# Kernel optimization log

Measured on AMD Instinct MI355X. Metric: run time of the kernel, lower is better.

Reference implementation:

```python
import jax, jax.numpy as jnp
import numpy as np

START_TAG = 2
STOP_TAG = 3
NEG = -10000.0


def _lstm_dir(x, w_ih, w_hh, b_ih, b_hh, h0, c0):
    """Single-direction LSTM over x:[T,F]. PyTorch gate order i,f,g,o."""
    xp = x @ w_ih.T + b_ih  # [T, 4H] - big GEMM done once

    def step(carry, xt):
        h, c = carry
        g = xt + h @ w_hh.T + b_hh
        i, f, gg, o = jnp.split(g, 4)
        c = jax.nn.sigmoid(f) * c + jax.nn.sigmoid(i) * jnp.tanh(gg)
        h = jax.nn.sigmoid(o) * jnp.tanh(c)
        return (h, c), h

    _, hs = jax.lax.scan(step, (h0, c0), xp)
    return hs  # [T, H]


def _viterbi(feats, transitions):
    # feats: [T, n_tags]; transitions[next, prev]
    n = transitions.shape[0]
    init = jnp.full((n,), NEG, feats.dtype).at[START_TAG].set(0.0)

    def step(fv, feat):
        scores = fv[None, :] + transitions          # [next, prev]
        bptr = jnp.argmax(scores, axis=1)           # best prev per next
        return jnp.max(scores, axis=1) + feat, bptr

    fv, bptrs = jax.lax.scan(step, init, feats)
    terminal = fv + transitions[STOP_TAG]
    best = jnp.argmax(terminal)
    score = terminal[best]

    def back(tag, bp):
        return bp[tag], tag  # emit tag at step t, carry tag at t-1

    _, path = jax.lax.scan(back, best, bptrs, reverse=True)
    return score, path  # scalar, [T] int32


def setup_inputs() -> dict:
    key = jax.random.key(0)
    T, F, H = 4096, 1024, 2048
    H2 = H // 2
    NTAG = 4
    ks = jax.random.split(key, 16)
    s_ih = 1.0 / np.sqrt(H2)

    def u(k, shape, s):
        return jax.random.uniform(k, shape, jnp.float32, -s, s)

    transitions = jax.random.normal(ks[13], (NTAG, NTAG), jnp.float32)
    transitions = transitions.at[START_TAG, :].set(NEG)
    transitions = transitions.at[:, STOP_TAG].set(NEG)

    return {
        "sentence": jax.random.normal(ks[0], (T, F), jnp.float32),
        "h0": jax.random.normal(ks[1], (2, 1, H2), jnp.float32),
        "c0": jax.random.normal(ks[2], (2, 1, H2), jnp.float32),
        "w_ih_f": u(ks[3], (4 * H2, F), s_ih),
        "w_hh_f": u(ks[4], (4 * H2, H2), s_ih),
        "b_ih_f": u(ks[5], (4 * H2,), s_ih),
        "b_hh_f": u(ks[6], (4 * H2,), s_ih),
        "w_ih_b": u(ks[7], (4 * H2, F), s_ih),
        "w_hh_b": u(ks[8], (4 * H2, H2), s_ih),
        "b_ih_b": u(ks[9], (4 * H2,), s_ih),
        "b_hh_b": u(ks[10], (4 * H2,), s_ih),
        "w_tag": u(ks[11], (NTAG, H), 1.0 / np.sqrt(H)),
        "b_tag": u(ks[12], (NTAG,), 1.0 / np.sqrt(H)),
        "transitions": transitions,
    }


def reference(sentence, h0, c0, w_ih_f, w_hh_f, b_ih_f, b_hh_f,
              w_ih_b, w_hh_b, b_ih_b, b_hh_b, w_tag, b_tag, transitions):
    # Bidirectional LSTM, batch=1 (torch stacks directions on dim 0 of h0/c0)
    h_fwd = _lstm_dir(sentence, w_ih_f, w_hh_f, b_ih_f, b_hh_f, h0[0, 0], c0[0, 0])
    h_bwd = _lstm_dir(sentence[::-1], w_ih_b, w_hh_b, b_ih_b, b_hh_b, h0[1, 0], c0[1, 0])[::-1]
    lstm_out = jnp.concatenate([h_fwd, h_bwd], axis=-1)  # [T, hidden_dim]
    feats = lstm_out @ w_tag.T + b_tag                    # [T, 4]
    score, path = _viterbi(feats, transitions)
    return score, path
```

## Files before the change

### kernel.cpp

```cpp
#include <hip/hip_runtime.h>
#include <cstddef>
#include <cstdint>

#define T_LEN 4096
#define FDIM  1024
#define H2DIM 1024
#define GDIM  4096

#define NEGV (-10000.0f)
#define START_TAG 2
#define STOP_TAG 3

#define XP_OFF      ((size_t)0)
#define XP_BYTES    ((size_t)2 * T_LEN * GDIM * 4)
#define HIST_OFF    (XP_OFF + XP_BYTES)
#define HIST_BYTES  ((size_t)T_LEN * 2048 * 4)
#define FEATS_OFF   (HIST_OFF + HIST_BYTES)
#define FEATS_BYTES ((size_t)T_LEN * 4 * 4)
#define SLOTS_OFF   (FEATS_OFF + FEATS_BYTES)
#define SLOTS_BYTES ((size_t)2 * 2 * 1024 * 8)
#define WS_NEED     (SLOTS_OFF + SLOTS_BYTES)

#define XB_OFF      (HIST_OFF)
#define WBF_OFF     (HIST_OFF + (size_t)8  * 1024 * 1024)
#define WBB_OFF     (HIST_OFF + (size_t)16 * 1024 * 1024)

__device__ __forceinline__ float sigm(float x) { return 1.0f / (1.0f + expf(-x)); }

__device__ __forceinline__ unsigned short f2bf(float f) {
    unsigned u = __float_as_uint(f);
    return (unsigned short)((u + 0x7FFFu + ((u >> 16) & 1u)) >> 16);
}

__device__ __forceinline__ unsigned compose4(unsigned A, unsigned B) {
    unsigned r = 0;
    #pragma unroll
    for (int c = 0; c < 4; ++c) {
        const unsigned b = (B >> (8 * c)) & 3u;
        const unsigned a = (A >> (8 * b)) & 3u;
        r |= a << (8 * c);
    }
    return r;
}

typedef short  bf16x8 __attribute__((ext_vector_type(8)));
typedef float  f32x4  __attribute__((ext_vector_type(4)));

__global__ __launch_bounds__(256)
void conv_bf16(const float* __restrict__ src, unsigned short* __restrict__ dst, int n4)
{
    int i = blockIdx.x * 256 + threadIdx.x;
    const int stride = gridDim.x * 256;
    for (; i < n4; i += stride) {
        const float4 v = ((const float4*)src)[i];
        ushort4 o;
        o.x = f2bf(v.x); o.y = f2bf(v.y); o.z = f2bf(v.z); o.w = f2bf(v.w);
        ((ushort4*)dst)[i] = o;
    }
}

__global__ __launch_bounds__(64)
void xp_gemm_mfma(const unsigned short* __restrict__ xb,
                  const unsigned short* __restrict__ wb_f,
                  const unsigned short* __restrict__ wb_b,
                  const float* __restrict__ bi_f, const float* __restrict__ bh_f,
                  const float* __restrict__ bi_b, const float* __restrict__ bh_b,
                  float* __restrict__ xp)
{
    const int lane = threadIdx.x;
    const int j0   = blockIdx.x * 64;
    const int t0   = blockIdx.y * 64;
    const int dir  = blockIdx.z;
    const unsigned short* __restrict__ wb = dir ? wb_b : wb_f;
    const float* __restrict__ bi = dir ? bi_b : bi_f;
    const float* __restrict__ bh = dir ? bh_b : bh_f;

    const int r  = lane & 15;
    const int kg = lane >> 4;

    const unsigned short* arow[4];
    const unsigned short* brow[4];
    #pragma unroll
    for (int s = 0; s < 4; ++s) {
        const int tg = t0 + s * 16 + r;
        const int sr = dir ? (T_LEN - 1 - tg) : tg;
        arow[s] = xb + (size_t)sr * FDIM + kg * 8;
        brow[s] = wb + (size_t)(j0 + s * 16 + r) * FDIM + kg * 8;
    }

    f32x4 acc[4][4];
    #pragma unroll
    for (int sm = 0; sm < 4; ++sm)
        #pragma unroll
        for (int sn = 0; sn < 4; ++sn)
            acc[sm][sn] = (f32x4){0.f, 0.f, 0.f, 0.f};

    for (int k0 = 0; k0 < FDIM; k0 += 32) {
        bf16x8 a[4], b[4];
        #pragma unroll
        for (int s = 0; s < 4; ++s) {
            a[s] = *(const bf16x8*)(arow[s] + k0);
            b[s] = *(const bf16x8*)(brow[s] + k0);
        }
        #pragma unroll
        for (int sm = 0; sm < 4; ++sm)
            #pragma unroll
            for (int sn = 0; sn < 4; ++sn)
                acc[sm][sn] = __builtin_amdgcn_mfma_f32_16x16x32_bf16(
                                  a[sm], b[sn], acc[sm][sn], 0, 0, 0);
    }

    float* __restrict__ xpd = xp + (size_t)dir * T_LEN * GDIM;
    #pragma unroll
    for (int sn = 0; sn < 4; ++sn) {
        const int col  = j0 + sn * 16 + r;
        const float bv = bi[col] + bh[col];
        #pragma unroll
        for (int sm = 0; sm < 4; ++sm) {
            #pragma unroll
            for (int j = 0; j < 4; ++j) {
                const int row = t0 + sm * 16 + kg * 4 + j;
                xpd[(size_t)row * GDIM + col] = acc[sm][sn][j] + bv;
            }
        }
    }
}

__global__ __launch_bounds__(256, 1)
void lstm_scan(const float* __restrict__ xp,
               const float* __restrict__ h0,
               const float* __restrict__ c0,
               const float* __restrict__ whh_f,
               const float* __restrict__ whh_b,
               float* __restrict__ hist,
               unsigned long long* __restrict__ slots)
{
    __shared__ float wsl[32][1024];
    __shared__ float hbuf[1024];
    __shared__ float gsh[32];

    const int tid = threadIdx.x;
    const int b   = blockIdx.x;
    const int dir = b & 1;
    const int bi  = b >> 1;
    const int u0  = bi * 8;
    const int rg  = tid >> 5;
    const int kc  = tid & 31;
    const int lrb = rg * 4;

    const float* __restrict__ whh = dir ? whh_b : whh_f;
    const size_t xpbase = (size_t)dir * T_LEN * GDIM;

    for (int lr = 0; lr < 32; ++lr) {
        const int grow = ((lr >> 3) << 10) + u0 + (lr & 7);
        *(float4*)&wsl[lr][tid * 4] = *(const float4*)&whh[(size_t)grow * H2DIM + tid * 4];
    }
    *(float4*)&hbuf[tid * 4] = *(const float4*)&h0[dir * H2DIM + tid * 4];
    float creg = 0.f;
    if (tid < 8) creg = c0[dir * H2DIM + u0 + tid];

    int grows[4];
    #pragma unroll
    for (int j = 0; j < 4; ++j) {
        const int lr = lrb + j;
        grows[j] = ((lr >> 3) << 10) + u0 + (lr & 7);
    }
    float xpc[4] = {0.f, 0.f, 0.f, 0.f};
    if (kc == 0) {
        #pragma unroll
        for (int j = 0; j < 4; ++j) xpc[j] = xp[xpbase + grows[j]];
    }
    __syncthreads();

    int budget = 4000000;

    for (int t = 0; t < T_LEN; ++t) {
        float xpn[4] = {0.f, 0.f, 0.f, 0.f};
        const int tnx = (t + 1 < T_LEN) ? (t + 1) : t;
        if (kc == 0) {
            #pragma unroll
            for (int j = 0; j < 4; ++j) xpn[j] = xp[xpbase + (size_t)tnx * GDIM + grows[j]];
        }

        float p0 = 0.f, p1 = 0.f, p2 = 0.f, p3 = 0.f;
        #pragma unroll
        for (int s = 0; s < 8; ++s) {
            const int ko = s * 128 + kc * 4;
            const float4 hv = *(const float4*)&hbuf[ko];
            const float4 w0 = *(const float4*)&wsl[lrb + 0][ko];
            const float4 w1 = *(const float4*)&wsl[lrb + 1][ko];
            const float4 w2 = *(const float4*)&wsl[lrb + 2][ko];
            const float4 w3 = *(const float4*)&wsl[lrb + 3][ko];
            p0 += w0.x*hv.x + w0.y*hv.y + w0.z*hv.z + w0.w*hv.w;
            p1 += w1.x*hv.x + w1.y*hv.y + w1.z*hv.z + w1.w*hv.w;
            p2 += w2.x*hv.x + w2.y*hv.y + w2.z*hv.z + w2.w*hv.w;
            p3 += w3.x*hv.x + w3.y*hv.y + w3.z*hv.z + w3.w*hv.w;
        }
        #pragma unroll
        for (int m = 16; m >= 1; m >>= 1) {
            p0 += __shfl_xor(p0, m);
            p1 += __shfl_xor(p1, m);
            p2 += __shfl_xor(p2, m);
            p3 += __shfl_xor(p3, m);
        }
        if (kc == 0) {
            gsh[lrb + 0] = p0 + xpc[0];
            gsh[lrb + 1] = p1 + xpc[1];
            gsh[lrb + 2] = p2 + xpc[2];
            gsh[lrb + 3] = p3 + xpc[3];
        }
        __syncthreads();

        if (tid < 8) {
            const float gi = gsh[tid];
            const float gf = gsh[8 + tid];
            const float gg = gsh[16 + tid];
            const float go = gsh[24 + tid];
            const float c  = sigm(gf) * creg + sigm(gi) * tanhf(gg);
            const float h  = sigm(go) * tanhf(c);
            creg = c;
            const int tg = dir ? (T_LEN - 1 - t) : t;
            hist[(size_t)tg * 2048 + dir * H2DIM + u0 + tid] = h;
            const unsigned long long pack =
                ((unsigned long long)(unsigned)(t + 1) << 32) |
                (unsigned long long)__float_as_uint(h);
            __hip_atomic_store(&slots[((size_t)((t + 1) & 1) * 2 + dir) * H2DIM + u0 + tid],
                               pack, __ATOMIC_RELAXED, __HIP_MEMORY_SCOPE_AGENT);
        }

        if (t + 1 < T_LEN) {
            const unsigned want = (unsigned)(t + 1);
            unsigned long long* sb = &slots[((size_t)((t + 1) & 1) * 2 + dir) * H2DIM + tid * 4];
            unsigned long long v0 = 0, v1 = 0, v2 = 0, v3 = 0;
            bool g0 = false, g1 = false, g2 = false, g3 = false;
            for (;;) {
                if (!g0) v0 = __hip_atomic_load(&sb[0], __ATOMIC_RELAXED, __HIP_MEMORY_SCOPE_AGENT);
                if (!g1) v1 = __hip_atomic_load(&sb[1], __ATOMIC_RELAXED, __HIP_MEMORY_SCOPE_AGENT);
                if (!g2) v2 = __hip_atomic_load(&sb[2], __ATOMIC_RELAXED, __HIP_MEMORY_SCOPE_AGENT);
                if (!g3) v3 = __hip_atomic_load(&sb[3], __ATOMIC_RELAXED, __HIP_MEMORY_SCOPE_AGENT);
                g0 = g0 || ((unsigned)(v0 >> 32) == want);
                g1 = g1 || ((unsigned)(v1 >> 32) == want);
                g2 = g2 || ((unsigned)(v2 >> 32) == want);
                g3 = g3 || ((unsigned)(v3 >> 32) == want);
                if (g0 && g1 && g2 && g3) break;
                if (--budget <= 0) break;
                __builtin_amdgcn_s_sleep(1);
            }
            float4 hv;
            hv.x = __uint_as_float((unsigned)v0);
            hv.y = __uint_as_float((unsigned)v1);
            hv.z = __uint_as_float((unsigned)v2);
            hv.w = __uint_as_float((unsigned)v3);
            *(float4*)&hbuf[tid * 4] = hv;
        }
        __syncthreads();
        if (kc == 0) { xpc[0] = xpn[0]; xpc[1] = xpn[1]; xpc[2] = xpn[2]; xpc[3] = xpn[3]; }
    }
}

__global__ __launch_bounds__(256)
void feats_kernel(const float* __restrict__ hist,
                  const float* __restrict__ w_tag,
                  const float* __restrict__ b_tag,
                  float* __restrict__ feats)
{
    const int t = blockIdx.x;
    const int tid = threadIdx.x;
    const float* __restrict__ hrow = hist + (size_t)t * 2048 + tid * 8;
    const float4 ha = *(const float4*)&hrow[0];
    const float4 hb = *(const float4*)&hrow[4];
    float p[4];
    #pragma unroll
    for (int n = 0; n < 4; ++n) {
        const float* __restrict__ wr = w_tag + n * 2048 + tid * 8;
        const float4 wa = *(const float4*)&wr[0];
        const float4 wb = *(const float4*)&wr[4];
        p[n] = ha.x*wa.x + ha.y*wa.y + ha.z*wa.z + ha.w*wa.w
             + hb.x*wb.x + hb.y*wb.y + hb.z*wb.z + hb.w*wb.w;
    }
    #pragma unroll
    for (int m = 32; m >= 1; m >>= 1) {
        #pragma unroll
        for (int n = 0; n < 4; ++n) p[n] += __shfl_down(p[n], m);
    }
    __shared__ float red[4][4];
    const int wv = tid >> 6;
    if ((tid & 63) == 0) {
        #pragma unroll
        for (int n = 0; n < 4; ++n) red[n][wv] = p[n];
    }
    __syncthreads();
    if (tid < 4)
        feats[(size_t)t * 4 + tid] = red[tid][0] + red[tid][1] + red[tid][2] + red[tid][3] + b_tag[tid];
}

__global__ __launch_bounds__(256)
void viterbi_kernel(const float* __restrict__ feats,
                    const float* __restrict__ trans,
                    float* __restrict__ out)
{
    __shared__ float fsh[T_LEN * 4];
    __shared__ unsigned bp[T_LEN];
    __shared__ unsigned lmap[256];
    __shared__ unsigned smap[256];
    __shared__ int bestsh;
    const int tid = threadIdx.x;
    for (int i = tid; i < T_LEN; i += 256)
        *(float4*)&fsh[i * 4] = *(const float4*)&feats[(size_t)i * 4];
    __syncthreads();

    if (tid == 0) {
        float tr[16];
        #pragma unroll
        for (int i = 0; i < 16; ++i) tr[i] = trans[i];
        float fv[4] = {NEGV, NEGV, NEGV, NEGV};
        fv[START_TAG] = 0.0f;
        for (int t0 = 0; t0 < T_LEN; t0 += 8) {
            float4 f8[8];
            #pragma unroll
            for (int j = 0; j < 8; ++j) f8[j] = *(const float4*)&fsh[(t0 + j) * 4];
            #pragma unroll
            for (int j = 0; j < 8; ++j) {
                const float ft[4] = {f8[j].x, f8[j].y, f8[j].z, f8[j].w};
                float nf[4]; unsigned pb = 0;
                #pragma unroll
                for (int n = 0; n < 4; ++n) {
                    float m = fv[0] + tr[n * 4 + 0]; int bsel = 0;
                    #pragma unroll
                    for (int p = 1; p < 4; ++p) {
                        const float s = fv[p] + tr[n * 4 + p];
                        if (s > m) { m = s; bsel = p; }
                    }
                    nf[n] = m + ft[n];
                    pb |= (unsigned)bsel << (8 * n);
                }
                bp[t0 + j] = pb;
                fv[0] = nf[0]; fv[1] = nf[1]; fv[2] = nf[2]; fv[3] = nf[3];
            }
        }
        float bm = fv[0] + tr[STOP_TAG * 4 + 0]; int best = 0;
        #pragma unroll
        for (int p = 1; p < 4; ++p) {
            const float s = fv[p] + tr[STOP_TAG * 4 + p];
            if (s > bm) { bm = s; best = p; }
        }
        out[0] = bm;
        bestsh = best;
    }
    __syncthreads();

    const int c0 = tid * 16;
    unsigned L = bp[c0 + 15];
    #pragma unroll
    for (int j = 14; j >= 0; --j) L = compose4(bp[c0 + j], L);
    lmap[tid] = L;
    __syncthreads();
    if (tid == 0) {
        unsigned acc = 0x03020100u;
        for (int i = 255; i >= 0; --i) { smap[i] = acc; acc = compose4(lmap[i], acc); }
    }
    __syncthreads();
    unsigned carry = smap[tid];
    const int best = bestsh;
    for (int t = c0 + 15; t >= c0; --t) {
        out[1 + t] = (float)((carry >> (8 * best)) & 3u);
        carry = compose4(bp[t], carry);
    }
}

extern "C" void kernel_launch(void* const* d_in, const int* in_sizes, int n_in,
                              void* d_out, int out_size, void* d_ws, size_t ws_size,
                              hipStream_t stream) {
    const float* x      = (const float*)d_in[0];
    const float* h0     = (const float*)d_in[1];
    const float* c0     = (const float*)d_in[2];
    const float* w_ih_f = (const float*)d_in[3];
    const float* w_hh_f = (const float*)d_in[4];
    const float* b_ih_f = (const float*)d_in[5];
    const float* b_hh_f = (const float*)d_in[6];
    const float* w_ih_b = (const float*)d_in[7];
    const float* w_hh_b = (const float*)d_in[8];
    const float* b_ih_b = (const float*)d_in[9];
    const float* b_hh_b = (const float*)d_in[10];
    const float* w_tag  = (const float*)d_in[11];
    const float* b_tag  = (const float*)d_in[12];
    const float* trans  = (const float*)d_in[13];
    float* out = (float*)d_out;

    if (ws_size < WS_NEED) return;

    char* ws = (char*)d_ws;
    float* xp    = (float*)(ws + XP_OFF);
    float* hist  = (float*)(ws + HIST_OFF);
    float* feats = (float*)(ws + FEATS_OFF);
    unsigned long long* slots = (unsigned long long*)(ws + SLOTS_OFF);
    unsigned short* xb  = (unsigned short*)(ws + XB_OFF);
    unsigned short* wbf = (unsigned short*)(ws + WBF_OFF);
    unsigned short* wbb = (unsigned short*)(ws + WBB_OFF);

    hipMemsetAsync(slots, 0, SLOTS_BYTES, stream);

    const int n4 = (T_LEN * FDIM) / 4;
    conv_bf16<<<1024, 256, 0, stream>>>(x,      xb,  n4);
    conv_bf16<<<1024, 256, 0, stream>>>(w_ih_f, wbf, n4);
    conv_bf16<<<1024, 256, 0, stream>>>(w_ih_b, wbb, n4);

    xp_gemm_mfma<<<dim3(64, 64, 2), 64, 0, stream>>>(
        xb, wbf, wbb, b_ih_f, b_hh_f, b_ih_b, b_hh_b, xp);

    void* ka[] = { (void*)&xp, (void*)&h0, (void*)&c0, (void*)&w_hh_f, (void*)&w_hh_b,
                   (void*)&hist, (void*)&slots };
    hipLaunchCooperativeKernel((void*)lstm_scan, dim3(256), dim3(256), ka, 0, stream);

    feats_kernel<<<T_LEN, 256, 0, stream>>>(hist, w_tag, b_tag, feats);
    viterbi_kernel<<<1, 256, 0, stream>>>(feats, trans, out);
}
```

Baseline: 14.01 ms.

## Tile input-projection GEMM through LDS with 128x128 blocks and block swizzle

The bf16 MFMA GEMM for the input projection now uses 256-thread blocks computing 128x128 tiles, staging A and B k-slices in padded shared memory so that four waves share the loaded data. Before, each 64-thread block read its operands directly from global memory. A swizzled block index groups neighbouring tiles to improve L2 reuse. The cost is two barriers per k-step with no double buffering, and the GEMM is a small part of a runtime dominated by the sequential LSTM scan.

Result: no change. 13.80 ms (-1.5%).

```diff
diff --git a/kernel.cpp b/kernel.cpp
--- a/kernel.cpp
+++ b/kernel.cpp
@@ -59,7 +59,7 @@
     }
 }
 
-__global__ __launch_bounds__(64)
+__global__ __launch_bounds__(256)
 void xp_gemm_mfma(const unsigned short* __restrict__ xb,
                   const unsigned short* __restrict__ wb_f,
                   const unsigned short* __restrict__ wb_b,
@@ -67,10 +67,21 @@
                   const float* __restrict__ bi_b, const float* __restrict__ bh_b,
                   float* __restrict__ xp)
 {
-    const int lane = threadIdx.x;
-    const int j0   = blockIdx.x * 64;
-    const int t0   = blockIdx.y * 64;
-    const int dir  = blockIdx.z;
+    __shared__ unsigned short As[128][40];
+    __shared__ unsigned short Bs[128][40];
+
+    const int tid  = threadIdx.x;
+    const int lane = tid & 63;
+    const int wv   = tid >> 6;
+    const int wr   = (wv >> 1) * 64;
+    const int wc   = (wv & 1) * 64;
+    const int dir  = blockIdx.y;
+
+    const int bid = blockIdx.x;
+    const int swz = (bid & 7) * 128 + (bid >> 3);
+    const int t0  = (swz >> 5) * 128;
+    const int j0  = (swz & 31) * 128;
+
     const unsigned short* __restrict__ wb = dir ? wb_b : wb_f;
     const float* __restrict__ bi = dir ? bi_b : bi_f;
     const float* __restrict__ bh = dir ? bh_b : bh_f;
@@ -78,15 +89,15 @@
     const int r  = lane & 15;
     const int kg = lane >> 4;
 
-    const unsigned short* arow[4];
-    const unsigned short* brow[4];
-    #pragma unroll
-    for (int s = 0; s < 4; ++s) {
-        const int tg = t0 + s * 16 + r;
-        const int sr = dir ? (T_LEN - 1 - tg) : tg;
-        arow[s] = xb + (size_t)sr * FDIM + kg * 8;
-        brow[s] = wb + (size_t)(j0 + s * 16 + r) * FDIM + kg * 8;
-    }
+    const int srow = tid >> 2;
+    const int skp  = (tid & 3) * 8;
+
+    const int tgA0 = t0 + srow;
+    const int tgA1 = t0 + srow + 64;
+    const size_t arow0 = (size_t)(dir ? (T_LEN - 1 - tgA0) : tgA0) * FDIM;
+    const size_t arow1 = (size_t)(dir ? (T_LEN - 1 - tgA1) : tgA1) * FDIM;
+    const size_t brow0 = (size_t)(j0 + srow) * FDIM;
+    const size_t brow1 = (size_t)(j0 + srow + 64) * FDIM;
 
     f32x4 acc[4][4];
     #pragma unroll
@@ -95,12 +106,19 @@
         for (int sn = 0; sn < 4; ++sn)
             acc[sm][sn] = (f32x4){0.f, 0.f, 0.f, 0.f};
 
-    for (int k0 = 0; k0 < FDIM; k0 += 32) {
+    for (int kb = 0; kb < FDIM; kb += 32) {
+        __syncthreads();
+        *(bf16x8*)&As[srow     ][skp] = *(const bf16x8*)&xb[arow0 + kb + skp];
+        *(bf16x8*)&As[srow + 64][skp] = *(const bf16x8*)&xb[arow1 + kb + skp];
+        *(bf16x8*)&Bs[srow     ][skp] = *(const bf16x8*)&wb[brow0 + kb + skp];
+        *(bf16x8*)&Bs[srow + 64][skp] = *(const bf16x8*)&wb[brow1 + kb + skp];
+        __syncthreads();
+
         bf16x8 a[4], b[4];
         #pragma unroll
         for (int s = 0; s < 4; ++s) {
-            a[s] = *(const bf16x8*)(arow[s] + k0);
-            b[s] = *(const bf16x8*)(brow[s] + k0);
+            a[s] = *(const bf16x8*)&As[wr + s * 16 + r][kg * 8];
+            b[s] = *(const bf16x8*)&Bs[wc + s * 16 + r][kg * 8];
         }
         #pragma unroll
         for (int sm = 0; sm < 4; ++sm)
@@ -113,13 +131,13 @@
     float* __restrict__ xpd = xp + (size_t)dir * T_LEN * GDIM;
     #pragma unroll
     for (int sn = 0; sn < 4; ++sn) {
-        const int col  = j0 + sn * 16 + r;
+        const int col  = j0 + wc + sn * 16 + r;
         const float bv = bi[col] + bh[col];
         #pragma unroll
         for (int sm = 0; sm < 4; ++sm) {
             #pragma unroll
             for (int j = 0; j < 4; ++j) {
-                const int row = t0 + sm * 16 + kg * 4 + j;
+                const int row = t0 + wr + sm * 16 + kg * 4 + j;
                 xpd[(size_t)row * GDIM + col] = acc[sm][sn][j] + bv;
             }
         }
@@ -405,7 +423,7 @@
     conv_bf16<<<1024, 256, 0, stream>>>(w_ih_f, wbf, n4);
     conv_bf16<<<1024, 256, 0, stream>>>(w_ih_b, wbb, n4);
 
-    xp_gemm_mfma<<<dim3(64, 64, 2), 64, 0, stream>>>(
+    xp_gemm_mfma<<<dim3(1024, 2), 256, 0, stream>>>(
         xb, wbf, wbb, b_ih_f, b_hh_f, b_ih_b, b_hh_b, xp);
 
     void* ka[] = { (void*)&xp, (void*)&h0, (void*)&c0, (void*)&w_hh_f, (void*)&w_hh_b,
```
